# Kernel tuning notes

Measured on AMD Instinct MI355X. Metric: run time of the kernel, lower is better.

The kernel has to match this reference:

```python
import jax, jax.numpy as jnp
import numpy as np

B, N, IN_DIM = 64, 4096, 128
D = 128          # slot_size
S = 7            # num_slots
ITERS = 3
HID = 256        # mlp_hdim
EPS = 1e-8       # renorm epsilon
LN_EPS = 1e-5    # torch LayerNorm default


def _ln(x, g, b):
    m = jnp.mean(x, axis=-1, keepdims=True)
    v = jnp.mean((x - m) ** 2, axis=-1, keepdims=True)
    return (x - m) * jax.lax.rsqrt(v + LN_EPS) * g + b


def setup_inputs() -> dict:
    key = jax.random.key(0)
    ks = jax.random.split(key, 16)
    s = 0.02
    return {
        "x": jax.random.normal(ks[0], (B, N, IN_DIM), jnp.float32),
        "noise": jax.random.normal(ks[1], (B, S, D), jnp.float32),
        "Wq": jax.random.normal(ks[2], (D, D), jnp.float32) * s,
        "Wk": jax.random.normal(ks[3], (D, IN_DIM), jnp.float32) * s,
        "Wv": jax.random.normal(ks[4], (D, IN_DIM), jnp.float32) * s,
        "ln_in_g": jnp.ones((IN_DIM,), jnp.float32),
        "ln_in_b": jnp.zeros((IN_DIM,), jnp.float32),
        "ln_slots_g": jnp.ones((D,), jnp.float32),
        "ln_slots_b": jnp.zeros((D,), jnp.float32),
        "ln_mlp_g": jnp.ones((D,), jnp.float32),
        "ln_mlp_b": jnp.zeros((D,), jnp.float32),
        "W_ih": jax.random.normal(ks[5], (3 * D, D), jnp.float32) * s,
        "W_hh": jax.random.normal(ks[6], (3 * D, D), jnp.float32) * s,
        "b_ih": jnp.zeros((3 * D,), jnp.float32),
        "b_hh": jnp.zeros((3 * D,), jnp.float32),
        "W1": jax.random.normal(ks[7], (HID, D), jnp.float32) * s,
        "b1": jnp.zeros((HID,), jnp.float32),
        "W2": jax.random.normal(ks[8], (D, HID), jnp.float32) * s,
        "b2": jnp.zeros((D,), jnp.float32),
        "mu": jax.random.normal(ks[9], (1, 1, D), jnp.float32) * s,
        "logsigma": jax.random.normal(ks[10], (1, D), jnp.float32) * s,
    }


def reference(x, noise, Wq, Wk, Wv, ln_in_g, ln_in_b, ln_slots_g, ln_slots_b,
              ln_mlp_g, ln_mlp_b, W_ih, W_hh, b_ih, b_hh, W1, b1, W2, b2,
              mu, logsigma):
    xn = _ln(x, ln_in_g, ln_in_b)              # (B,N,IN)
    k = xn @ Wk.T                              # (B,N,D)
    v = xn @ Wv.T                              # (B,N,D)

    scale = jax.nn.softplus(logsigma)[None] + 1e-5   # (1,1,D)
    slots = mu + scale * noise                 # rsample, (B,S,D)

    def gru(u, h):
        gx = u @ W_ih.T + b_ih                 # (B*S, 3D)
        gh = h @ W_hh.T + b_hh
        xr, xz, xn_ = jnp.split(gx, 3, axis=-1)
        hr, hz, hn = jnp.split(gh, 3, axis=-1)
        r = jax.nn.sigmoid(xr + hr)
        z = jax.nn.sigmoid(xz + hz)
        n = jnp.tanh(xn_ + r * hn)
        return (1.0 - z) * n + z * h

    inv_sqrt_d = D ** -0.5
    for _ in range(ITERS):
        slots_prev = slots
        sn = _ln(slots, ln_slots_g, ln_slots_b)
        q = sn @ Wq.T                          # (B,S,D)
        scores = inv_sqrt_d * jnp.einsum('bnd,bsd->bns', k, q)
        attn = jax.nn.softmax(scores, axis=-1)           # over slots
        attn = attn + EPS
        attn = attn / jnp.sum(attn, axis=1, keepdims=True)  # renorm over inputs
        updates = jnp.einsum('bns,bnd->bsd', attn, v)    # (B,S,D)
        h = gru(updates.reshape(-1, D), slots_prev.reshape(-1, D))
        slots = h.reshape(x.shape[0], S, D)
        slots = _ln(slots, ln_mlp_g, ln_mlp_b)
        slots = slots + (jax.nn.relu(slots @ W1.T + b1) @ W2.T + b2)
    return slots
```

## Files before the change

kernel.cpp:

```cpp
#include <hip/hip_runtime.h>
#include <hip/hip_bf16.h>
#include <stdint.h>

#define B_ 64
#define N_ 4096
#define D_ 128
#define S_ 7
#define EPS_ 1e-8f
#define LN_EPS_ 1e-5f

typedef float  f32x4  __attribute__((ext_vector_type(4)));
typedef __bf16 bf16x8 __attribute__((ext_vector_type(8)));

__device__ __forceinline__ uint16_t f2bfbits(float f) {
    uint32_t x = __float_as_uint(f);
    return (uint16_t)((x + 0x7fffu + ((x >> 16) & 1u)) >> 16);
}
__device__ __forceinline__ uint32_t pk2(float a, float b) {
    return (uint32_t)f2bfbits(a) | ((uint32_t)f2bfbits(b) << 16);
}
__device__ __forceinline__ bf16x8 ldfrag_w(const float* wp) {
    f32x4 w0 = *(const f32x4*)wp, w1 = *(const f32x4*)(wp + 4);
    bf16x8 r;
    #pragma unroll
    for (int c = 0; c < 4; ++c) { r[c] = (__bf16)w0[c]; r[4 + c] = (__bf16)w1[c]; }
    return r;
}

__global__ void k_prep(const float* __restrict__ noise, const float* __restrict__ Wk,
                       const float* __restrict__ Wv, const float* __restrict__ mu,
                       const float* __restrict__ logsigma,
                       uint16_t* __restrict__ Wsw, float* __restrict__ slots,
                       uint16_t* __restrict__ qbf) {
    int tid = blockIdx.x * 256 + threadIdx.x;
    if (tid < B_ * 16 * D_) qbf[tid] = 0;
    if (tid < B_ * S_ * D_) {
        int d = tid & (D_ - 1);
        float sc = log1pf(__expf(logsigma[d])) + 1e-5f;
        slots[tid] = mu[d] + sc * noise[tid];
    }
    if (tid < 32768) {
        int j = tid & 7, ch = tid >> 3;
        int lane = ch & 63, k0 = (ch >> 6) & 3, wt = (ch >> 8) & 7, h = ch >> 11;
        int row = wt * 16 + (lane & 15);
        int col = k0 * 32 + (lane >> 4) * 8 + j;
        float w = h ? Wv[row * 128 + col] : Wk[row * 128 + col];
        Wsw[tid] = f2bfbits(w);
    }
}

__global__ __launch_bounds__(512) void k_proj(
    const float* __restrict__ x, const uint16_t* __restrict__ Wsw,
    const float* __restrict__ lng, const float* __restrict__ lnb,
    uint16_t* __restrict__ kbf, uint16_t* __restrict__ vbf_t) {
    __shared__ __align__(16) uint16_t wlds[16384];
    const int t = threadIdx.x, wv = t >> 6, lane = t & 63;
    const int lm = lane & 15, qd = lane >> 4;
    const long row0 = (long)blockIdx.x * 128;
    const int b = (int)(row0 >> 12);
    const int nloc = (int)(row0 & 4095);

    uint4 wst[4];
    #pragma unroll
    for (int i = 0; i < 4; ++i)
        wst[i] = *(const uint4*)(Wsw + (i * 512 + t) * 8);

    const long xrow = row0 + wv * 16 + lm;
    const float* xp = x + xrow * 128 + qd * 8;
    f32x4 xa[8];
    #pragma unroll
    for (int k0 = 0; k0 < 4; ++k0) {
        xa[2 * k0]     = *(const f32x4*)(xp + k0 * 32);
        xa[2 * k0 + 1] = *(const f32x4*)(xp + k0 * 32 + 4);
    }
    #pragma unroll
    for (int i = 0; i < 4; ++i)
        *(uint4*)(wlds + (i * 512 + t) * 8) = wst[i];

    float s = 0.f, sq = 0.f;
    #pragma unroll
    for (int i = 0; i < 8; ++i)
        #pragma unroll
        for (int c = 0; c < 4; ++c) { float v = xa[i][c]; s += v; sq += v * v; }
    s  += __shfl_xor(s, 16);  s  += __shfl_xor(s, 32);
    sq += __shfl_xor(sq, 16); sq += __shfl_xor(sq, 32);
    float mean = s * (1.0f / 128.0f);
    float var  = sq * (1.0f / 128.0f) - mean * mean;
    float rs   = rsqrtf(var + LN_EPS_);

    bf16x8 xf[4];
    #pragma unroll
    for (int k0 = 0; k0 < 4; ++k0) {
        const float* gp = lng + k0 * 32 + qd * 8;
        const float* bp = lnb + k0 * 32 + qd * 8;
        f32x4 g0 = *(const f32x4*)(gp), g1 = *(const f32x4*)(gp + 4);
        f32x4 b0 = *(const f32x4*)(bp), b1 = *(const f32x4*)(bp + 4);
        #pragma unroll
        for (int c = 0; c < 4; ++c) {
            xf[k0][c]     = (__bf16)((xa[2 * k0][c]     - mean) * rs * g0[c] + b0[c]);
            xf[k0][4 + c] = (__bf16)((xa[2 * k0 + 1][c] - mean) * rs * g1[c] + b1[c]);
        }
    }
    __syncthreads();

    #pragma unroll
    for (int mt = 0; mt < 8; ++mt) {
        f32x4 acc = {0.f, 0.f, 0.f, 0.f};
        #pragma unroll
        for (int k0 = 0; k0 < 4; ++k0) {
            bf16x8 wf = *(const bf16x8*)(wlds + ((mt * 4 + k0) * 64 + lane) * 8);
            acc = __builtin_amdgcn_mfma_f32_16x16x32_bf16(wf, xf[k0], acc, 0, 0, 0);
        }
        uint2 st; st.x = pk2(acc[0], acc[1]); st.y = pk2(acc[2], acc[3]);
        *(uint2*)(kbf + (row0 + wv * 16 + lm) * 128 + mt * 16 + qd * 4) = st;
    }
    __syncthreads();

    #pragma unroll
    for (int i = 0; i < 4; ++i)
        wst[i] = *(const uint4*)(Wsw + 16384 + (i * 512 + t) * 8);
    #pragma unroll
    for (int i = 0; i < 4; ++i)
        *(uint4*)(wlds + (i * 512 + t) * 8) = wst[i];
    __syncthreads();

    #pragma unroll
    for (int nt = 0; nt < 8; ++nt) {
        f32x4 acc = {0.f, 0.f, 0.f, 0.f};
        #pragma unroll
        for (int k0 = 0; k0 < 4; ++k0) {
            bf16x8 wf = *(const bf16x8*)(wlds + ((nt * 4 + k0) * 64 + lane) * 8);
            acc = __builtin_amdgcn_mfma_f32_16x16x32_bf16(xf[k0], wf, acc, 0, 0, 0);
        }
        uint2 st; st.x = pk2(acc[0], acc[1]); st.y = pk2(acc[2], acc[3]);
        *(uint2*)(vbf_t + ((long)(b * 128 + nt * 16 + lm)) * 4096 + nloc + wv * 16 + qd * 4) = st;
    }
}

__global__ __launch_bounds__(128) void k_slotq(
    const float* __restrict__ slots, const float* __restrict__ Wq,
    const float* __restrict__ g, const float* __restrict__ bt,
    uint16_t* __restrict__ qbf) {
    int row = blockIdx.x;
    int b = row / 7, s = row - b * 7;
    int t = threadIdx.x;
    __shared__ float sn[128];
    __shared__ float red[2];
    float v = slots[row * 128 + t];
    float sv = v;
    #pragma unroll
    for (int m = 1; m < 64; m <<= 1) sv += __shfl_xor(sv, m);
    if ((t & 63) == 0) red[t >> 6] = sv;
    __syncthreads();
    float mean = (red[0] + red[1]) * (1.0f / 128.0f);
    __syncthreads();
    float dv = v - mean, sq = dv * dv;
    #pragma unroll
    for (int m = 1; m < 64; m <<= 1) sq += __shfl_xor(sq, m);
    if ((t & 63) == 0) red[t >> 6] = sq;
    __syncthreads();
    float var = (red[0] + red[1]) * (1.0f / 128.0f);
    sn[t] = dv * rsqrtf(var + LN_EPS_) * g[t] + bt[t];
    __syncthreads();
    const float4* wr = (const float4*)(Wq + t * 128);
    float acc = 0.f;
    #pragma unroll 8
    for (int j = 0; j < 32; ++j) {
        float4 w = wr[j];
        float4 s4 = *(const float4*)(sn + 4 * j);
        acc += w.x * s4.x + w.y * s4.y + w.z * s4.z + w.w * s4.w;
    }
    qbf[(b * 16 + s) * 128 + t] = f2bfbits(acc * 0.08838834764831843f);
}

__global__ __launch_bounds__(512) void k_attn(
    const uint16_t* __restrict__ kbf, const uint16_t* __restrict__ vbf_t,
    const uint16_t* __restrict__ qbf,
    float* __restrict__ upart, float* __restrict__ cpart) {
    __shared__ __align__(16) uint16_t als[8][1024];
    __shared__ __align__(16) float part[8][7][132];
    __shared__ float bsum[8][8];
    const int t = threadIdx.x, wv = t >> 6, lane = t & 63;
    const int lm = lane & 15, qd = lane >> 4;
    const int b = blockIdx.x >> 3, chunk = blockIdx.x & 7;
    const int rb = chunk * 512 + wv * 64;
    const long gbase = (long)b * N_ + rb;

    bf16x8 bq[4];
    #pragma unroll
    for (int k0 = 0; k0 < 4; ++k0)
        bq[k0] = *(const bf16x8*)(qbf + b * 2048 + lm * 128 + k0 * 32 + qd * 8);

    float csl = 0.f;
    #pragma unroll
    for (int mt = 0; mt < 4; ++mt) {
        f32x4 acc = {0.f, 0.f, 0.f, 0.f};
        long rr = gbase + mt * 16;
        #pragma unroll
        for (int k0 = 0; k0 < 4; ++k0) {
            bf16x8 a = *(const bf16x8*)(kbf + (rr + lm) * 128 + k0 * 32 + qd * 8);
            acc = __builtin_amdgcn_mfma_f32_16x16x32_bf16(a, bq[k0], acc, 0, 0, 0);
        }
        uint16_t pb[4];
        #pragma unroll
        for (int r = 0; r < 4; ++r) {
            float sc = acc[r];
            float scm = (lm < 7) ? sc : -1e30f;
            #pragma unroll
            for (int m = 1; m < 16; m <<= 1) scm = fmaxf(scm, __shfl_xor(scm, m));
            float e = (lm < 7) ? __expf(sc - scm) : 0.f;
            float tot = e;
            #pragma unroll
            for (int m = 1; m < 16; m <<= 1) tot += __shfl_xor(tot, m);
            float a_ = e / tot + EPS_;
            if (lm < 7) csl += a_;
            pb[r] = f2bfbits(a_);
        }
        int elem = (mt >> 1) * 512 + (((mt & 1) * 2 + (qd >> 1)) * 16 + lm) * 8 + (qd & 1) * 4;
        uint2 pw; pw.x = (uint32_t)pb[0] | ((uint32_t)pb[1] << 16);
        pw.y = (uint32_t)pb[2] | ((uint32_t)pb[3] << 16);
        *(uint2*)(&als[wv][elem]) = pw;
    }
    csl += __shfl_xor(csl, 16); csl += __shfl_xor(csl, 32);
    if (lane < 7) bsum[wv][lane] = csl;
    __syncthreads();

    bf16x8 afr0 = *(const bf16x8*)(&als[wv][lane * 8]);
    bf16x8 afr1 = *(const bf16x8*)(&als[wv][512 + lane * 8]);
    f32x4 uacc[8];
    #pragma unroll
    for (int i = 0; i < 8; ++i) uacc[i] = (f32x4){0.f, 0.f, 0.f, 0.f};
    #pragma unroll
    for (int nt = 0; nt < 8; ++nt) {
        const uint16_t* vp = vbf_t + ((long)(b * 128 + nt * 16 + lm)) * 4096 + rb;
        bf16x8 v0 = *(const bf16x8*)(vp + qd * 8);
        bf16x8 v1 = *(const bf16x8*)(vp + 32 + qd * 8);
        uacc[nt] = __builtin_amdgcn_mfma_f32_16x16x32_bf16(v0, afr0, uacc[nt], 0, 0, 0);
        uacc[nt] = __builtin_amdgcn_mfma_f32_16x16x32_bf16(v1, afr1, uacc[nt], 0, 0, 0);
    }
    if (lm < 7) {
        #pragma unroll
        for (int nt = 0; nt < 8; ++nt)
            *(f32x4*)&part[wv][lm][nt * 16 + qd * 4] = uacc[nt];
    }
    __syncthreads();
    if (t < 128) {
        #pragma unroll
        for (int s = 0; s < 7; ++s) {
            float v = 0.f;
            #pragma unroll
            for (int w = 0; w < 8; ++w) v += part[w][s][t];
            upart[((b * 8 + chunk) * 7 + s) * 128 + t] = v;
        }
    }
    if (t < 7) {
        float c = 0.f;
        #pragma unroll
        for (int w = 0; w < 8; ++w) c += bsum[w][t];
        cpart[(b * 8 + chunk) * 7 + t] = c;
    }
}

__global__ __launch_bounds__(256) void k_fused(
    const float* __restrict__ upart, const float* __restrict__ cpart,
    float* __restrict__ slots,
    const float* __restrict__ Wih, const float* __restrict__ Whh,
    const float* __restrict__ bih, const float* __restrict__ bhh,
    const float* __restrict__ gm, const float* __restrict__ bm,
    const float* __restrict__ W1, const float* __restrict__ b1,
    const float* __restrict__ W2, const float* __restrict__ b2,
    const float* __restrict__ Wq, const float* __restrict__ lsg,
    const float* __restrict__ lsb,
    uint16_t* __restrict__ qbf, float* __restrict__ dst, int hasq) {
    __shared__ float uf[16][132];
    __shared__ float hf[16][132];
    __shared__ float slf[16][132];
    __shared__ float hidl[16][264];
    __shared__ float glg[7][776];
    __shared__ float csl[7];
    const int b = blockIdx.x;
    const int t = threadIdx.x, wv = t >> 6, lane = t & 63;
    const int lm = lane & 15, qd = lane >> 4;

    if (t < 7) {
        float c = 0.f;
        #pragma unroll
        for (int i = 0; i < 8; ++i) c += cpart[(b * 8 + i) * 7 + t];
        csl[t] = c;
    }
    __syncthreads();
    for (int idx = t; idx < 896; idx += 256) {
        int s = idx >> 7, d = idx & 127;
        float acc = 0.f;
        #pragma unroll
        for (int i = 0; i < 8; ++i) acc += upart[((b * 8 + i) * 7 + s) * 128 + d];
        uf[s][d] = acc / csl[s];
        hf[s][d] = slots[(b * 7 + s) * 128 + d];
    }
    __syncthreads();

    bf16x8 au[4], ah[4];
    #pragma unroll
    for (int k0 = 0; k0 < 4; ++k0)
        #pragma unroll
        for (int j = 0; j < 8; ++j) {
            au[k0][j] = (__bf16)uf[lm][k0 * 32 + qd * 8 + j];
            ah[k0][j] = (__bf16)hf[lm][k0 * 32 + qd * 8 + j];
        }

    {
        const int ih = (wv < 2);
        const float* W = ih ? Wih : Whh;
        const int base = ih ? 0 : 384;
        const int w2 = wv & 1;
        #pragma unroll
        for (int i = 0; i < 12; ++i) {
            int o0 = (w2 * 12 + i) * 16;
            f32x4 acc = {0.f, 0.f, 0.f, 0.f};
            #pragma unroll
            for (int k0 = 0; k0 < 4; ++k0) {
                bf16x8 bf = ldfrag_w(W + (o0 + lm) * 128 + k0 * 32 + qd * 8);
                acc = __builtin_amdgcn_mfma_f32_16x16x32_bf16(ih ? au[k0] : ah[k0], bf, acc, 0, 0, 0);
            }
            #pragma unroll
            for (int r = 0; r < 4; ++r) {
                int s = qd * 4 + r;
                if (s < 7) glg[s][base + o0 + lm] = acc[r];
            }
        }
    }
    __syncthreads();

    for (int idx = t; idx < 896; idx += 256) {
        int s = idx >> 7, d = idx & 127;
        float xr = glg[s][d] + bih[d];
        float xz = glg[s][128 + d] + bih[128 + d];
        float xn = glg[s][256 + d] + bih[256 + d];
        float hr = glg[s][384 + d] + bhh[d];
        float hz = glg[s][512 + d] + bhh[128 + d];
        float hnn = glg[s][640 + d] + bhh[256 + d];
        float r = 1.f / (1.f + __expf(-(xr + hr)));
        float z = 1.f / (1.f + __expf(-(xz + hz)));
        float n = tanhf(xn + r * hnn);
        uf[s][d] = (1.f - z) * n + z * hf[s][d];
    }
    __syncthreads();

    for (int s = wv; s < 7; s += 4) {
        float a0 = uf[s][2 * lane], a1 = uf[s][2 * lane + 1];
        float sm = a0 + a1, sq = a0 * a0 + a1 * a1;
        #pragma unroll
        for (int m = 1; m < 64; m <<= 1) { sm += __shfl_xor(sm, m); sq += __shfl_xor(sq, m); }
        float mean = sm * (1.0f / 128.0f);
        float var = sq * (1.0f / 128.0f) - mean * mean;
        float rs = rsqrtf(var + LN_EPS_);
        slf[s][2 * lane]     = (a0 - mean) * rs * gm[2 * lane] + bm[2 * lane];
        slf[s][2 * lane + 1] = (a1 - mean) * rs * gm[2 * lane + 1] + bm[2 * lane + 1];
    }
    __syncthreads();

    bf16x8 as_[4];
    #pragma unroll
    for (int k0 = 0; k0 < 4; ++k0)
        #pragma unroll
        for (int j = 0; j < 8; ++j) as_[k0][j] = (__bf16)slf[lm][k0 * 32 + qd * 8 + j];
    #pragma unroll
    for (int i = 0; i < 4; ++i) {
        int o0 = (wv * 4 + i) * 16;
        f32x4 acc = {0.f, 0.f, 0.f, 0.f};
        #pragma unroll
        for (int k0 = 0; k0 < 4; ++k0) {
            bf16x8 bf = ldfrag_w(W1 + (o0 + lm) * 128 + k0 * 32 + qd * 8);
            acc = __builtin_amdgcn_mfma_f32_16x16x32_bf16(as_[k0], bf, acc, 0, 0, 0);
        }
        #pragma unroll
        for (int r = 0; r < 4; ++r) {
            int s = qd * 4 + r;
            if (s < 7) hidl[s][o0 + lm] = fmaxf(acc[r] + b1[o0 + lm], 0.f);
        }
    }
    __syncthreads();

    bf16x8 ahd[8];
    #pragma unroll
    for (int k0 = 0; k0 < 8; ++k0)
        #pragma unroll
        for (int j = 0; j < 8; ++j) ahd[k0][j] = (__bf16)hidl[lm][k0 * 32 + qd * 8 + j];
    #pragma unroll
    for (int i = 0; i < 2; ++i) {
        int o0 = (wv * 2 + i) * 16;
        f32x4 acc = {0.f, 0.f, 0.f, 0.f};
        #pragma unroll
        for (int k0 = 0; k0 < 8; ++k0) {
            bf16x8 bf = ldfrag_w(W2 + (o0 + lm) * 256 + k0 * 32 + qd * 8);
            acc = __builtin_amdgcn_mfma_f32_16x16x32_bf16(ahd[k0], bf, acc, 0, 0, 0);
        }
        #pragma unroll
        for (int r = 0; r < 4; ++r) {
            int s = qd * 4 + r;
            if (s < 7) {
                float v = slf[s][o0 + lm] + acc[r] + b2[o0 + lm];
                hf[s][o0 + lm] = v;
                dst[(b * 7 + s) * 128 + o0 + lm] = v;
            }
        }
    }
    if (hasq) {
        __syncthreads();
        for (int s = wv; s < 7; s += 4) {
            float a0 = hf[s][2 * lane], a1 = hf[s][2 * lane + 1];
            float sm = a0 + a1, sq = a0 * a0 + a1 * a1;
            #pragma unroll
            for (int m = 1; m < 64; m <<= 1) { sm += __shfl_xor(sm, m); sq += __shfl_xor(sq, m); }
            float mean = sm * (1.0f / 128.0f);
            float var = sq * (1.0f / 128.0f) - mean * mean;
            float rs = rsqrtf(var + LN_EPS_);
            uf[s][2 * lane]     = (a0 - mean) * rs * lsg[2 * lane] + lsb[2 * lane];
            uf[s][2 * lane + 1] = (a1 - mean) * rs * lsg[2 * lane + 1] + lsb[2 * lane + 1];
        }
        __syncthreads();
        bf16x8 an[4];
        #pragma unroll
        for (int k0 = 0; k0 < 4; ++k0)
            #pragma unroll
            for (int j = 0; j < 8; ++j) an[k0][j] = (__bf16)uf[lm][k0 * 32 + qd * 8 + j];
        #pragma unroll
        for (int i = 0; i < 2; ++i) {
            int o0 = (wv * 2 + i) * 16;
            f32x4 acc = {0.f, 0.f, 0.f, 0.f};
            #pragma unroll
            for (int k0 = 0; k0 < 4; ++k0) {
                bf16x8 bf = ldfrag_w(Wq + (o0 + lm) * 128 + k0 * 32 + qd * 8);
                acc = __builtin_amdgcn_mfma_f32_16x16x32_bf16(an[k0], bf, acc, 0, 0, 0);
            }
            #pragma unroll
            for (int r = 0; r < 4; ++r) {
                int s = qd * 4 + r;
                if (s < 7)
                    qbf[(b * 16 + s) * 128 + o0 + lm] = f2bfbits(acc[r] * 0.08838834764831843f);
            }
        }
    }
}

extern "C" void kernel_launch(void* const* d_in, const int* in_sizes, int n_in,
                              void* d_out, int out_size, void* d_ws, size_t ws_size,
                              hipStream_t stream) {
    const float* x    = (const float*)d_in[0];
    const float* nz   = (const float*)d_in[1];
    const float* Wq   = (const float*)d_in[2];
    const float* Wk   = (const float*)d_in[3];
    const float* Wv   = (const float*)d_in[4];
    const float* ling = (const float*)d_in[5];
    const float* linb = (const float*)d_in[6];
    const float* lsg  = (const float*)d_in[7];
    const float* lsb  = (const float*)d_in[8];
    const float* lmg  = (const float*)d_in[9];
    const float* lmb  = (const float*)d_in[10];
    const float* Wih  = (const float*)d_in[11];
    const float* Whh  = (const float*)d_in[12];
    const float* bih  = (const float*)d_in[13];
    const float* bhh  = (const float*)d_in[14];
    const float* W1   = (const float*)d_in[15];
    const float* b1   = (const float*)d_in[16];
    const float* W2   = (const float*)d_in[17];
    const float* b2   = (const float*)d_in[18];
    const float* mu   = (const float*)d_in[19];
    const float* lsig = (const float*)d_in[20];

    char* wsb = (char*)d_ws;
    uint16_t* kbf   = (uint16_t*)(wsb);
    uint16_t* vbf_t = (uint16_t*)(wsb + (size_t)67108864);
    uint16_t* Wsw   = (uint16_t*)(wsb + (size_t)134217728);
    uint16_t* qbf   = (uint16_t*)(wsb + (size_t)134283264);
    float*    slots = (float*)  (wsb + (size_t)134545408);
    float*    upart = (float*)  (wsb + (size_t)134774784);
    float*    cpart = (float*)  (wsb + (size_t)136609792);

    k_prep<<<512, 256, 0, stream>>>(nz, Wk, Wv, mu, lsig, Wsw, slots, qbf);
    k_proj<<<2048, 512, 0, stream>>>(x, Wsw, ling, linb, kbf, vbf_t);
    k_slotq<<<448, 128, 0, stream>>>(slots, Wq, lsg, lsb, qbf);
    for (int it = 0; it < 3; ++it) {
        float* dst = (it == 2) ? (float*)d_out : slots;
        k_attn<<<512, 512, 0, stream>>>(kbf, vbf_t, qbf, upart, cpart);
        k_fused<<<64, 256, 0, stream>>>(upart, cpart, slots, Wih, Whh, bih, bhh,
                                        lmg, lmb, W1, b1, W2, b2, Wq, lsg, lsb,
                                        qbf, dst, (it < 2) ? 1 : 0);
    }
}
```

Baseline: 427.8 us.

## Stage projection outputs through LDS for coalesced stores; fuse slot-q into prep

The K and V projection results are first written into a padded LDS buffer and then copied to global memory as contiguous 16-byte-per-lane rows, replacing the scattered 8-byte stores (especially the strided transposed V writes). Both weight halves are prefetched into registers up front, so the second weight load no longer sits between the two GEMM phases. The separate slot LayerNorm plus query-projection kernel is merged into the prep kernel, removing one launch. The cost is extra LDS (about 33 KB more per block), which may lower occupancy, plus more registers and an extra barrier.

After: 443.3 us. +3.6%, slower.

```diff
diff --git a/kernel.cpp b/kernel.cpp
--- a/kernel.cpp
+++ b/kernel.cpp
@@ -27,17 +27,54 @@
     return r;
 }
 
-__global__ void k_prep(const float* __restrict__ noise, const float* __restrict__ Wk,
-                       const float* __restrict__ Wv, const float* __restrict__ mu,
-                       const float* __restrict__ logsigma,
-                       uint16_t* __restrict__ Wsw, float* __restrict__ slots,
-                       uint16_t* __restrict__ qbf) {
-    int tid = blockIdx.x * 256 + threadIdx.x;
-    if (tid < B_ * 16 * D_) qbf[tid] = 0;
-    if (tid < B_ * S_ * D_) {
-        int d = tid & (D_ - 1);
-        float sc = log1pf(__expf(logsigma[d])) + 1e-5f;
-        slots[tid] = mu[d] + sc * noise[tid];
+__global__ __launch_bounds__(256) void k_prep(
+    const float* __restrict__ noise, const float* __restrict__ Wk,
+    const float* __restrict__ Wv, const float* __restrict__ mu,
+    const float* __restrict__ logsigma, const float* __restrict__ Wq,
+    const float* __restrict__ lsg, const float* __restrict__ lsb,
+    uint16_t* __restrict__ Wsw, float* __restrict__ slots,
+    uint16_t* __restrict__ qbf) {
+    const int t = threadIdx.x;
+    const int tid = blockIdx.x * 256 + t;
+    __shared__ float sn[128];
+    __shared__ float red[2];
+    {
+        int row = blockIdx.x;
+        int b = row / 7, s = row - b * 7;
+        bool act = t < 128;
+        float v = 0.f;
+        if (act) {
+            float sc = log1pf(__expf(logsigma[t])) + 1e-5f;
+            v = mu[t] + sc * noise[row * 128 + t];
+            slots[row * 128 + t] = v;
+        }
+        float sv = act ? v : 0.f;
+        #pragma unroll
+        for (int m = 1; m < 64; m <<= 1) sv += __shfl_xor(sv, m);
+        if (act && (t & 63) == 0) red[t >> 6] = sv;
+        __syncthreads();
+        float mean = (red[0] + red[1]) * (1.0f / 128.0f);
+        __syncthreads();
+        float dv = act ? (v - mean) : 0.f;
+        float sq = dv * dv;
+        #pragma unroll
+        for (int m = 1; m < 64; m <<= 1) sq += __shfl_xor(sq, m);
+        if (act && (t & 63) == 0) red[t >> 6] = sq;
+        __syncthreads();
+        float var = (red[0] + red[1]) * (1.0f / 128.0f);
+        if (act) sn[t] = dv * rsqrtf(var + LN_EPS_) * lsg[t] + lsb[t];
+        __syncthreads();
+        if (act) {
+            const float4* wr = (const float4*)(Wq + t * 128);
+            float acc = 0.f;
+            #pragma unroll 8
+            for (int j = 0; j < 32; ++j) {
+                float4 w = wr[j];
+                float4 s4 = *(const float4*)(sn + 4 * j);
+                acc += w.x * s4.x + w.y * s4.y + w.z * s4.z + w.w * s4.w;
+            }
+            qbf[(b * 16 + s) * 128 + t] = f2bfbits(acc * 0.08838834764831843f);
+        }
     }
     if (tid < 32768) {
         int j = tid & 7, ch = tid >> 3;
@@ -47,6 +84,11 @@
         float w = h ? Wv[row * 128 + col] : Wk[row * 128 + col];
         Wsw[tid] = f2bfbits(w);
     }
+    if (tid < 73728) {
+        int bb = tid / 1152, rem = tid - bb * 1152;
+        int s = 7 + (rem >> 7), d = rem & 127;
+        qbf[(bb * 16 + s) * 128 + d] = 0;
+    }
 }
 
 __global__ __launch_bounds__(512) void k_proj(
@@ -54,16 +96,19 @@
     const float* __restrict__ lng, const float* __restrict__ lnb,
     uint16_t* __restrict__ kbf, uint16_t* __restrict__ vbf_t) {
     __shared__ __align__(16) uint16_t wlds[16384];
+    __shared__ __align__(16) uint16_t cb[128 * 132];
     const int t = threadIdx.x, wv = t >> 6, lane = t & 63;
     const int lm = lane & 15, qd = lane >> 4;
     const long row0 = (long)blockIdx.x * 128;
     const int b = (int)(row0 >> 12);
     const int nloc = (int)(row0 & 4095);
 
-    uint4 wst[4];
-    #pragma unroll
-    for (int i = 0; i < 4; ++i)
-        wst[i] = *(const uint4*)(Wsw + (i * 512 + t) * 8);
+    uint4 w0[4], w1[4];
+    #pragma unroll
+    for (int i = 0; i < 4; ++i) {
+        w0[i] = *(const uint4*)(Wsw + (i * 512 + t) * 8);
+        w1[i] = *(const uint4*)(Wsw + 16384 + (i * 512 + t) * 8);
+    }
 
     const long xrow = row0 + wv * 16 + lm;
     const float* xp = x + xrow * 128 + qd * 8;
@@ -75,7 +120,7 @@
     }
     #pragma unroll
     for (int i = 0; i < 4; ++i)
-        *(uint4*)(wlds + (i * 512 + t) * 8) = wst[i];
+        *(uint4*)(wlds + (i * 512 + t) * 8) = w0[i];
 
     float s = 0.f, sq = 0.f;
     #pragma unroll
@@ -112,16 +157,26 @@
             acc = __builtin_amdgcn_mfma_f32_16x16x32_bf16(wf, xf[k0], acc, 0, 0, 0);
         }
         uint2 st; st.x = pk2(acc[0], acc[1]); st.y = pk2(acc[2], acc[3]);
-        *(uint2*)(kbf + (row0 + wv * 16 + lm) * 128 + mt * 16 + qd * 4) = st;
-    }
-    __syncthreads();
-
+        *(uint2*)(cb + (wv * 16 + lm) * 132 + mt * 16 + qd * 4) = st;
+    }
+    __syncthreads();
+
+    {
+        int r = t >> 2, c0 = (t & 3) * 32;
+        const uint16_t* src = cb + r * 132 + c0;
+        uint16_t* dst = kbf + (row0 + r) * 128 + c0;
+        uint4 d0 = *(const uint4*)(src);
+        uint4 d1 = *(const uint4*)(src + 8);
+        uint4 d2 = *(const uint4*)(src + 16);
+        uint4 d3 = *(const uint4*)(src + 24);
+        *(uint4*)(dst)      = d0;
+        *(uint4*)(dst + 8)  = d1;
+        *(uint4*)(dst + 16) = d2;
+        *(uint4*)(dst + 24) = d3;
+    }
     #pragma unroll
     for (int i = 0; i < 4; ++i)
-        wst[i] = *(const uint4*)(Wsw + 16384 + (i * 512 + t) * 8);
-    #pragma unroll
-    for (int i = 0; i < 4; ++i)
-        *(uint4*)(wlds + (i * 512 + t) * 8) = wst[i];
+        *(uint4*)(wlds + (i * 512 + t) * 8) = w1[i];
     __syncthreads();
 
     #pragma unroll
@@ -133,44 +188,23 @@
             acc = __builtin_amdgcn_mfma_f32_16x16x32_bf16(xf[k0], wf, acc, 0, 0, 0);
         }
         uint2 st; st.x = pk2(acc[0], acc[1]); st.y = pk2(acc[2], acc[3]);
-        *(uint2*)(vbf_t + ((long)(b * 128 + nt * 16 + lm)) * 4096 + nloc + wv * 16 + qd * 4) = st;
-    }
-}
-
-__global__ __launch_bounds__(128) void k_slotq(
-    const float* __restrict__ slots, const float* __restrict__ Wq,
-    const float* __restrict__ g, const float* __restrict__ bt,
-    uint16_t* __restrict__ qbf) {
-    int row = blockIdx.x;
-    int b = row / 7, s = row - b * 7;
-    int t = threadIdx.x;
-    __shared__ float sn[128];
-    __shared__ float red[2];
-    float v = slots[row * 128 + t];
-    float sv = v;
-    #pragma unroll
-    for (int m = 1; m < 64; m <<= 1) sv += __shfl_xor(sv, m);
-    if ((t & 63) == 0) red[t >> 6] = sv;
-    __syncthreads();
-    float mean = (red[0] + red[1]) * (1.0f / 128.0f);
-    __syncthreads();
-    float dv = v - mean, sq = dv * dv;
-    #pragma unroll
-    for (int m = 1; m < 64; m <<= 1) sq += __shfl_xor(sq, m);
-    if ((t & 63) == 0) red[t >> 6] = sq;
-    __syncthreads();
-    float var = (red[0] + red[1]) * (1.0f / 128.0f);
-    sn[t] = dv * rsqrtf(var + LN_EPS_) * g[t] + bt[t];
-    __syncthreads();
-    const float4* wr = (const float4*)(Wq + t * 128);
-    float acc = 0.f;
-    #pragma unroll 8
-    for (int j = 0; j < 32; ++j) {
-        float4 w = wr[j];
-        float4 s4 = *(const float4*)(sn + 4 * j);
-        acc += w.x * s4.x + w.y * s4.y + w.z * s4.z + w.w * s4.w;
-    }
-    qbf[(b * 16 + s) * 128 + t] = f2bfbits(acc * 0.08838834764831843f);
+        *(uint2*)(cb + (nt * 16 + lm) * 132 + wv * 16 + qd * 4) = st;
+    }
+    __syncthreads();
+
+    {
+        int d = t >> 2, c0 = (t & 3) * 32;
+        const uint16_t* src = cb + d * 132 + c0;
+        uint16_t* dst = vbf_t + ((long)(b * 128 + d)) * 4096 + nloc + c0;
+        uint4 d0 = *(const uint4*)(src);
+        uint4 d1 = *(const uint4*)(src + 8);
+        uint4 d2 = *(const uint4*)(src + 16);
+        uint4 d3 = *(const uint4*)(src + 24);
+        *(uint4*)(dst)      = d0;
+        *(uint4*)(dst + 8)  = d1;
+        *(uint4*)(dst + 16) = d2;
+        *(uint4*)(dst + 24) = d3;
+    }
 }
 
 __global__ __launch_bounds__(512) void k_attn(
@@ -477,9 +511,9 @@
     float*    upart = (float*)  (wsb + (size_t)134774784);
     float*    cpart = (float*)  (wsb + (size_t)136609792);
 
-    k_prep<<<512, 256, 0, stream>>>(nz, Wk, Wv, mu, lsig, Wsw, slots, qbf);
+    k_prep<<<448, 256, 0, stream>>>(nz, Wk, Wv, mu, lsig, Wq, lsg, lsb,
+                                    Wsw, slots, qbf);
     k_proj<<<2048, 512, 0, stream>>>(x, Wsw, ling, linb, kbf, vbf_t);
-    k_slotq<<<448, 128, 0, stream>>>(slots, Wq, lsg, lsb, qbf);
     for (int it = 0; it < 3; ++it) {
         float* dst = (it == 2) ? (float*)d_out : slots;
         k_attn<<<512, 512, 0, stream>>>(kbf, vbf_t, qbf, upart, cpart);
```
